# Kernel tuning notes

Measured on AMD Instinct MI355X. Metric: run time of the kernel, lower is better.

The kernel has to match this reference:

```python
import jax, jax.numpy as jnp
import numpy as np

D = 512       # d_model
DC = 768      # d_context
H = 8         # heads
DFF = 2048    # d_ff
EPS = 1e-6


def _ln(x, g, b):
    mu = jnp.mean(x, axis=-1, keepdims=True)
    var = jnp.mean(jnp.square(x - mu), axis=-1, keepdims=True)
    return (x - mu) * jax.lax.rsqrt(var + EPS) * g + b


def _mha(q_in, k_in, v_in, mask, wq, bq, wk, bk, wv, bv, wo, bo):
    # q_in [B,Sq,D], k_in/v_in [B,Sk,D], mask [B,Sq,Sk] (nonzero -> blocked)
    B, Sq, _ = q_in.shape
    Sk = k_in.shape[1]
    dh = D // H
    q = (q_in @ wq + bq).reshape(B, Sq, H, dh)
    k = (k_in @ wk + bk).reshape(B, Sk, H, dh)
    v = (v_in @ wv + bv).reshape(B, Sk, H, dh)
    scores = jnp.einsum('bqhd,bkhd->bhqk', q, k) / np.float32(np.sqrt(dh))
    scores = jnp.where(mask[:, None, :, :].astype(bool), jnp.float32(-1e18), scores)
    attn = jax.nn.softmax(scores, axis=-1)
    ctx = jnp.einsum('bhqk,bkhd->bqhd', attn, v).reshape(B, Sq, D)
    return ctx @ wo + bo


def _aggregate_chains(batch_size, ctx_out, chain_map, chain_mask):
    # ctx_out [TC,S,D]; keep positions where mask[:,:,0] is set, else -inf,
    # then max-pool chains belonging to the same example (segment max).
    keep = chain_mask[:, :, 0].astype(bool)[:, :, None]
    masked = jnp.where(keep, ctx_out, jnp.float32(-jnp.inf))
    out = jax.ops.segment_max(masked, chain_map, num_segments=batch_size)
    # replicate torch.where(out + 1 == out, 0, out): zeros out -inf entries
    return jnp.where(out + 1 == out, jnp.float32(0.0), out)


def _lin_params(key, din, dout):
    return jax.random.normal(key, (din, dout), jnp.float32) * 0.02, jnp.zeros((dout,), jnp.float32)


def setup_inputs() -> dict:
    key = jax.random.key(0)
    ks = jax.random.split(key, 20)
    B, S, TC, L = 16, 512, 128, 12
    inp = {}
    inp['inputs'] = jax.random.normal(ks[0], (B, S, D), jnp.float32)
    inp['attn_mask'] = jax.random.randint(ks[1], (B, S, S), 0, 2, jnp.int32)
    inp['chain_map'] = jax.random.randint(ks[2], (TC,), 0, B, jnp.int32)
    inp['span_embeddings'] = jax.random.normal(ks[3], (TC, L, DC), jnp.float32)
    inp['chain_mask'] = jax.random.randint(ks[4], (TC, S, L), 0, 2, jnp.int32)
    inp['ln_g'] = jnp.ones((D,), jnp.float32)
    inp['ln_b'] = jnp.zeros((D,), jnp.float32)
    inp['sa_wq'], inp['sa_bq'] = _lin_params(ks[5], D, D)
    inp['sa_wk'], inp['sa_bk'] = _lin_params(ks[6], D, D)
    inp['sa_wv'], inp['sa_bv'] = _lin_params(ks[7], D, D)
    inp['sa_wo'], inp['sa_bo'] = _lin_params(ks[8], D, D)
    inp['lc_w'], inp['lc_b'] = _lin_params(ks[9], DC, D)
    inp['ca_wq'], inp['ca_bq'] = _lin_params(ks[10], D, D)
    inp['ca_wk'], inp['ca_bk'] = _lin_params(ks[11], D, D)
    inp['ca_wv'], inp['ca_bv'] = _lin_params(ks[12], D, D)
    inp['ca_wo'], inp['ca_bo'] = _lin_params(ks[13], D, D)
    inp['g_w'], inp['g_b'] = _lin_params(ks[14], 2 * D, D)
    inp['ff_ln_g'] = jnp.ones((D,), jnp.float32)
    inp['ff_ln_b'] = jnp.zeros((D,), jnp.float32)
    inp['ff_w1'], inp['ff_b1'] = _lin_params(ks[15], D, DFF)
    inp['ff_w2'], inp['ff_b2'] = _lin_params(ks[16], DFF, D)
    return inp


def reference(inputs, attn_mask, chain_map, span_embeddings, chain_mask,
              ln_g, ln_b,
              sa_wq, sa_bq, sa_wk, sa_bk, sa_wv, sa_bv, sa_wo, sa_bo,
              lc_w, lc_b,
              ca_wq, ca_bq, ca_wk, ca_bk, ca_wv, ca_bv, ca_wo, ca_bo,
              g_w, g_b,
              ff_ln_g, ff_ln_b, ff_w1, ff_b1, ff_w2, ff_b2):
    B = inputs.shape[0]
    input_norm = _ln(inputs, ln_g, ln_b)
    attn_context = _mha(input_norm, input_norm, input_norm, attn_mask,
                        sa_wq, sa_bq, sa_wk, sa_bk, sa_wv, sa_bv, sa_wo, sa_bo)
    emb_transformed = span_embeddings @ lc_w + lc_b              # [TC,L,D]
    context_query = input_norm[chain_map]                         # [TC,S,D]
    ctx_out = _mha(context_query, emb_transformed, emb_transformed, chain_mask,
                   ca_wq, ca_bq, ca_wk, ca_bk, ca_wv, ca_bv, ca_wo, ca_bo)
    ctx_context = _aggregate_chains(B, ctx_out, chain_map, chain_mask)
    # SimpleGate
    z = jax.nn.sigmoid(jnp.concatenate((attn_context, ctx_context), axis=-1) @ g_w + g_b)
    gated = z * attn_context + (1.0 - z) * ctx_context
    out = gated + inputs  # dropout is identity at eval
    # PositionwiseFeedForward (pre-LN, residual)
    y = _ln(out, ff_ln_g, ff_ln_b)
    inter = jax.nn.relu(y @ ff_w1 + ff_b1)
    return inter @ ff_w2 + ff_b2 + out
```

## Files before the change

### kernel.cpp

```cpp
#include <hip/hip_runtime.h>
#include <hip/hip_bf16.h>
#include <math.h>

typedef float f32x4_t __attribute__((ext_vector_type(4)));
typedef __bf16 bf16x8_t __attribute__((ext_vector_type(8)));
typedef __bf16 bf16x4_t __attribute__((ext_vector_type(4)));

__device__ __forceinline__ void gload16(const void* g, void* l) {
  __builtin_amdgcn_global_load_lds((const __attribute__((address_space(1))) void*)g,
                                   (__attribute__((address_space(3))) void*)l, 16, 0, 0);
}

struct WDesc { const float* src; __bf16* hi; __bf16* lo; int K; int N; };
struct WPack { WDesc w[12]; };

__global__ __launch_bounds__(256) void prep_weights_kernel(WPack p) {
  WDesc d = p.w[blockIdx.y];
  const int tilesN = d.N >> 6;
  const int ntiles = (d.K >> 6) * tilesN;
  __shared__ float tile[64][65];
  const int tid = threadIdx.x;
  const int r = tid >> 4, cq = (tid & 15) << 2;
  const int c = tid >> 4, rq = (tid & 15) << 2;
  for (int t = blockIdx.x; t < ntiles; t += gridDim.x) {
    const int tk = t / tilesN, tn = t - tk * tilesN;
    const int k0 = tk << 6, n0 = tn << 6;
#pragma unroll
    for (int i = 0; i < 4; i++) {
      const float4 v = *reinterpret_cast<const float4*>(
          &d.src[(size_t)(k0 + r + i * 16) * d.N + n0 + cq]);
      tile[r + i * 16][cq] = v.x; tile[r + i * 16][cq + 1] = v.y;
      tile[r + i * 16][cq + 2] = v.z; tile[r + i * 16][cq + 3] = v.w;
    }
    __syncthreads();
#pragma unroll
    for (int i = 0; i < 4; i++) {
      const int cc = c + i * 16;
      const float v0 = tile[rq][cc], v1 = tile[rq + 1][cc];
      const float v2 = tile[rq + 2][cc], v3 = tile[rq + 3][cc];
      const __bf16 h0 = (__bf16)v0, h1 = (__bf16)v1, h2 = (__bf16)v2, h3 = (__bf16)v3;
      bf16x4_t hv = {h0, h1, h2, h3};
      bf16x4_t lv = {(__bf16)(v0 - (float)h0), (__bf16)(v1 - (float)h1),
                     (__bf16)(v2 - (float)h2), (__bf16)(v3 - (float)h3)};
      *reinterpret_cast<bf16x4_t*>(&d.hi[(size_t)(n0 + cc) * d.K + k0 + rq]) = hv;
      *reinterpret_cast<bf16x4_t*>(&d.lo[(size_t)(n0 + cc) * d.K + k0 + rq]) = lv;
    }
    __syncthreads();
  }
}

__global__ __launch_bounds__(256) void bias_cat_kernel(
    const float* __restrict__ b0, const float* __restrict__ b1,
    const float* __restrict__ b2, const float* __restrict__ b3,
    float* __restrict__ out) {
  const int t = blockIdx.x * 256 + threadIdx.x;
  const float* s = t < 512 ? b0 : t < 1024 ? b1 : t < 1536 ? b2 : b3;
  out[t] = s[t & 511];
}

__global__ __launch_bounds__(256) void split_kernel(
    const float* __restrict__ x, __bf16* __restrict__ h, __bf16* __restrict__ l, int nq) {
  const int i = blockIdx.x * 256 + threadIdx.x;
  if (i >= nq) return;
  const float4 v = reinterpret_cast<const float4*>(x)[i];
  const __bf16 h0 = (__bf16)v.x, h1 = (__bf16)v.y, h2 = (__bf16)v.z, h3 = (__bf16)v.w;
  bf16x4_t hv = {h0, h1, h2, h3};
  bf16x4_t lv = {(__bf16)(v.x - (float)h0), (__bf16)(v.y - (float)h1),
                 (__bf16)(v.z - (float)h2), (__bf16)(v.w - (float)h3)};
  reinterpret_cast<bf16x4_t*>(h)[i] = hv;
  reinterpret_cast<bf16x4_t*>(l)[i] = lv;
}

__global__ __launch_bounds__(256) void ln_split_kernel(
    const float* __restrict__ x, const float* __restrict__ g,
    const float* __restrict__ bb, __bf16* __restrict__ yh, __bf16* __restrict__ yl) {
  const int row = blockIdx.x * 4 + (threadIdx.x >> 6);
  const int lane = threadIdx.x & 63;
  const float* xr = x + (size_t)row * 512;
  float4 a = *reinterpret_cast<const float4*>(&xr[lane * 8]);
  float4 b4 = *reinterpret_cast<const float4*>(&xr[lane * 8 + 4]);
  float v[8] = {a.x, a.y, a.z, a.w, b4.x, b4.y, b4.z, b4.w};
  float s = 0.f;
#pragma unroll
  for (int j = 0; j < 8; j++) s += v[j];
#pragma unroll
  for (int off = 1; off < 64; off <<= 1) s += __shfl_xor(s, off);
  const float mean = s * (1.f / 512.f);
  float sq = 0.f;
#pragma unroll
  for (int j = 0; j < 8; j++) { v[j] -= mean; sq += v[j] * v[j]; }
#pragma unroll
  for (int off = 1; off < 64; off <<= 1) sq += __shfl_xor(sq, off);
  const float inv = rsqrtf(sq * (1.f / 512.f) + 1e-6f);
  bf16x8_t hv, lv;
#pragma unroll
  for (int j = 0; j < 8; j++) {
    const float o = v[j] * inv * g[lane * 8 + j] + bb[lane * 8 + j];
    const __bf16 h = (__bf16)o;
    hv[j] = h; lv[j] = (__bf16)(o - (float)h);
  }
  *reinterpret_cast<bf16x8_t*>(&yh[(size_t)row * 512 + lane * 8]) = hv;
  *reinterpret_cast<bf16x8_t*>(&yl[(size_t)row * 512 + lane * 8]) = lv;
}

template <int EPI>
__global__ __launch_bounds__(256, 2) void gemm2_kernel(
    const __bf16* __restrict__ A0h, const __bf16* __restrict__ A0l,
    const __bf16* __restrict__ A1h, const __bf16* __restrict__ A1l,
    int lda, int ksplit,
    const __bf16* __restrict__ Bh, const __bf16* __restrict__ Bl, int K,
    const float* __restrict__ bias,
    float* __restrict__ Cf, __bf16* __restrict__ Ch, __bf16* __restrict__ Cl,
    __bf16* __restrict__ C2h, __bf16* __restrict__ C2l,
    __bf16* __restrict__ C3h, __bf16* __restrict__ C3l,
    int ldc, size_t sec_stride,
    const __bf16* __restrict__ e0h, const __bf16* __restrict__ e0l,
    const __bf16* __restrict__ e1h, const __bf16* __restrict__ e1l,
    const float* __restrict__ e2) {
  __shared__ __bf16 lds[4][128][64];
  const int tid = threadIdx.x;
  const int wave = tid >> 6, lane = tid & 63;
  const int brow = blockIdx.y * 128, bcol = blockIdx.x * 128;
  const int wr = (wave >> 1) * 64, wc = (wave & 1) * 64;
  const int lr = lane & 15, hi = lane >> 4;
  const int s_row = lane >> 3;
  const int s_sc = (lane & 7) ^ s_row;
  const int tile_row = (wave < 2 ? brow : bcol) + s_row;

  f32x4_t acc[4][4] = {};

  for (int k0 = 0; k0 < K; k0 += 64) {
    const __bf16* ah = A0h; const __bf16* al = A0l; int kc = k0;
    if (k0 >= ksplit) { ah = A1h; al = A1l; kc = k0 - ksplit; }
    const __bf16* plane = wave == 0 ? ah : wave == 1 ? al : wave == 2 ? Bh : Bl;
    const int pl_lda = wave < 2 ? lda : K;
    const int pk = wave < 2 ? kc : k0;
    const __bf16* src = plane + (size_t)tile_row * pl_lda + pk + s_sc * 8;
#pragma unroll
    for (int i = 0; i < 16; i++)
      gload16(src + (size_t)i * 8 * pl_lda, &lds[wave][i * 8][0]);
    __syncthreads();
#pragma unroll
    for (int kk = 0; kk < 2; kk++) {
      bf16x8_t afh[4], afl[4], bfh[4], bfl[4];
#pragma unroll
      for (int m = 0; m < 4; m++) {
        const int row = wr + m * 16 + lr;
        const int ch = (kk * 4 + hi) ^ (row & 7);
        afh[m] = *(const bf16x8_t*)((const char*)&lds[0][0][0] + row * 128 + ch * 16);
        afl[m] = *(const bf16x8_t*)((const char*)&lds[1][0][0] + row * 128 + ch * 16);
      }
#pragma unroll
      for (int n = 0; n < 4; n++) {
        const int row = wc + n * 16 + lr;
        const int ch = (kk * 4 + hi) ^ (row & 7);
        bfh[n] = *(const bf16x8_t*)((const char*)&lds[2][0][0] + row * 128 + ch * 16);
        bfl[n] = *(const bf16x8_t*)((const char*)&lds[3][0][0] + row * 128 + ch * 16);
      }
#pragma unroll
      for (int m = 0; m < 4; m++)
#pragma unroll
        for (int n = 0; n < 4; n++) {
          acc[m][n] = __builtin_amdgcn_mfma_f32_16x16x32_bf16(afh[m], bfh[n], acc[m][n], 0, 0, 0);
          acc[m][n] = __builtin_amdgcn_mfma_f32_16x16x32_bf16(afh[m], bfl[n], acc[m][n], 0, 0, 0);
          acc[m][n] = __builtin_amdgcn_mfma_f32_16x16x32_bf16(afl[m], bfh[n], acc[m][n], 0, 0, 0);
        }
    }
    __syncthreads();
  }

#pragma unroll
  for (int m = 0; m < 4; m++) {
#pragma unroll
    for (int n = 0; n < 4; n++) {
      const int colg = bcol + wc + n * 16 + lr;
      const size_t cb = (size_t)(colg >> 9) * sec_stride + (colg & 511);
      const float bv = bias[colg];
#pragma unroll
      for (int r = 0; r < 4; r++) {
        const int row = brow + wr + m * 16 + hi * 4 + r;
        float v = acc[m][n][r] + bv;
        if constexpr (EPI == 0) {
          Cf[cb + (size_t)row * ldc] = v;
        } else if constexpr (EPI == 1) {
          const __bf16 h = (__bf16)v;
          Ch[cb + (size_t)row * ldc] = h;
          Cl[cb + (size_t)row * ldc] = (__bf16)(v - (float)h);
        } else if constexpr (EPI == 2) {
          v = fmaxf(v, 0.f);
          const __bf16 h = (__bf16)v;
          Ch[cb + (size_t)row * ldc] = h;
          Cl[cb + (size_t)row * ldc] = (__bf16)(v - (float)h);
        } else if constexpr (EPI == 3) {
          const float z = 1.f / (1.f + expf(-v));
          const size_t ei = (size_t)row * 512 + colg;
          const float a = (float)e0h[ei] + (float)e0l[ei];
          const float c = (float)e1h[ei] + (float)e1l[ei];
          Cf[cb + (size_t)row * ldc] = z * a + (1.f - z) * c + e2[ei];
        } else if constexpr (EPI == 4) {
          Cf[cb + (size_t)row * ldc] = v + e2[(size_t)row * 512 + colg];
        } else if constexpr (EPI == 5) {
          const int sec = colg >> 9, cc = colg & 511;
          const __bf16 h = (__bf16)v;
          const __bf16 lo = (__bf16)(v - (float)h);
          if (sec == 0)      { Ch[(size_t)row * 512 + cc] = h;  Cl[(size_t)row * 512 + cc] = lo; }
          else if (sec == 1) { C2h[(size_t)row * 512 + cc] = h; C2l[(size_t)row * 512 + cc] = lo; }
          else if (sec == 2) {
            const int bb2 = row >> 9, ss = row & 511, hh2 = cc >> 6, dv = cc & 63;
            const size_t va = ((size_t)((bb2 * 8 + hh2) * 64 + dv)) * 512 + ss;
            C3h[va] = h; C3l[va] = lo;
          } else {
            Cf[(size_t)row * 512 + cc] = v;
          }
        }
      }
    }
  }
}

__global__ __launch_bounds__(256, 2) void sa_attn_mfma_kernel(
    const __bf16* __restrict__ Qh_g, const __bf16* __restrict__ Ql_g,
    const __bf16* __restrict__ Kh_g, const __bf16* __restrict__ Kl_g,
    const __bf16* __restrict__ Vth_g, const __bf16* __restrict__ Vtl_g,
    const int* __restrict__ mask,
    __bf16* __restrict__ Oh, __bf16* __restrict__ Ol) {
  __shared__ __bf16 Qs[2][64][64];
  __shared__ __bf16 Ks[2][64][64];
  __shared__ __bf16 Vs[2][64][64];
  __shared__ __bf16 Ps[2][64][64];
  const int tid = threadIdx.x;
  const int wid = tid >> 6, lane = tid & 63;
  const int q0 = blockIdx.x * 64;
  const int h = blockIdx.y, b = blockIdx.z;
  const int lr = lane & 15, hi = lane >> 4;
  const int s_row = lane >> 3;
  const int s_sc = (lane & 7) ^ s_row;

  {
    const __bf16* qp = (wid < 2 ? Qh_g : Ql_g);
    const int pl = (wid < 2 ? 0 : 1);
    const int r0 = (wid & 1) * 32;
    const __bf16* src = qp + (size_t)(b * 512 + q0 + r0 + s_row) * 512 + h * 64 + s_sc * 8;
#pragma unroll
    for (int i = 0; i < 4; i++)
      gload16(src + (size_t)i * 8 * 512, &Qs[pl][r0 + i * 8][0]);
  }
  f32x4_t accO[4] = {};
  float m_[4], l_[4];
#pragma unroll
  for (int j = 0; j < 4; j++) { m_[j] = -INFINITY; l_[j] = 0.f; }

  for (int kt = 0; kt < 8; kt++) {
    const int k0 = kt * 64;
    __syncthreads();
    {
      const __bf16* plane = wid == 0 ? Kh_g : wid == 1 ? Kl_g : wid == 2 ? Vth_g : Vtl_g;
      size_t srow; int scol;
      if (wid < 2) { srow = (size_t)(b * 512 + k0 + s_row);          scol = h * 64; }
      else         { srow = (size_t)((b * 8 + h) * 64 + s_row);      scol = k0; }
      const __bf16* src = plane + srow * 512 + scol + s_sc * 8;
      __bf16* dst0 = (wid == 0) ? &Ks[0][0][0] : (wid == 1) ? &Ks[1][0][0]
                   : (wid == 2) ? &Vs[0][0][0] : &Vs[1][0][0];
#pragma unroll
      for (int i = 0; i < 8; i++)
        gload16(src + (size_t)i * 8 * 512, dst0 + i * 8 * 64);
    }
    __syncthreads();

    f32x4_t acc[4] = {};
#pragma unroll
    for (int kk = 0; kk < 2; kk++) {
      const int arow = wid * 16 + lr;
      const int ach = (kk * 4 + hi) ^ (arow & 7);
      bf16x8_t aqh = *(const bf16x8_t*)&Qs[0][arow][ach * 8];
      bf16x8_t aql = *(const bf16x8_t*)&Qs[1][arow][ach * 8];
#pragma unroll
      for (int n = 0; n < 4; n++) {
        const int brw = n * 16 + lr;
        const int bch = (kk * 4 + hi) ^ (brw & 7);
        bf16x8_t bkh = *(const bf16x8_t*)&Ks[0][brw][bch * 8];
        bf16x8_t bkl = *(const bf16x8_t*)&Ks[1][brw][bch * 8];
        acc[n] = __builtin_amdgcn_mfma_f32_16x16x32_bf16(aqh, bkh, acc[n], 0, 0, 0);
        acc[n] = __builtin_amdgcn_mfma_f32_16x16x32_bf16(aqh, bkl, acc[n], 0, 0, 0);
        acc[n] = __builtin_amdgcn_mfma_f32_16x16x32_bf16(aql, bkh, acc[n], 0, 0, 0);
      }
    }

    float p[4][4];
    const int qbase = b * 512 + q0 + wid * 16 + hi * 4;
#pragma unroll
    for (int j = 0; j < 4; j++) {
      float rowmax = -INFINITY;
#pragma unroll
      for (int n = 0; n < 4; n++) {
        const int mk = mask[(size_t)(qbase + j) * 512 + k0 + n * 16 + lr];
        const float sv = mk ? -1e18f : acc[n][j] * 0.125f;
        p[n][j] = sv;
        rowmax = fmaxf(rowmax, sv);
      }
#pragma unroll
      for (int off = 1; off <= 8; off <<= 1) rowmax = fmaxf(rowmax, __shfl_xor(rowmax, off));
      const float mnew = fmaxf(m_[j], rowmax);
      const float scale = expf(m_[j] - mnew);
      float rs = 0.f;
#pragma unroll
      for (int n = 0; n < 4; n++) { const float e = expf(p[n][j] - mnew); p[n][j] = e; rs += e; }
#pragma unroll
      for (int off = 1; off <= 8; off <<= 1) rs += __shfl_xor(rs, off);
      l_[j] = l_[j] * scale + rs;
      m_[j] = mnew;
#pragma unroll
      for (int nv = 0; nv < 4; nv++) accO[nv][j] *= scale;
    }

#pragma unroll
    for (int j = 0; j < 4; j++) {
      const int qrow = wid * 16 + hi * 4 + j;
#pragma unroll
      for (int n = 0; n < 4; n++) {
        const int col = n * 16 + lr;
        const int colp = ((((col >> 3) ^ (qrow & 7)) << 3) | (col & 7));
        const __bf16 ph = (__bf16)p[n][j];
        Ps[0][qrow][colp] = ph;
        Ps[1][qrow][colp] = (__bf16)(p[n][j] - (float)ph);
      }
    }

#pragma unroll
    for (int kk = 0; kk < 2; kk++) {
      const int arow = wid * 16 + lr;
      const int ach = (kk * 4 + hi) ^ (arow & 7);
      bf16x8_t aph = *(const bf16x8_t*)&Ps[0][arow][ach * 8];
      bf16x8_t apl = *(const bf16x8_t*)&Ps[1][arow][ach * 8];
#pragma unroll
      for (int nv = 0; nv < 4; nv++) {
        const int brw = nv * 16 + lr;
        const int bch = (kk * 4 + hi) ^ (brw & 7);
        bf16x8_t bvh = *(const bf16x8_t*)&Vs[0][brw][bch * 8];
        bf16x8_t bvl = *(const bf16x8_t*)&Vs[1][brw][bch * 8];
        accO[nv] = __builtin_amdgcn_mfma_f32_16x16x32_bf16(aph, bvh, accO[nv], 0, 0, 0);
        accO[nv] = __builtin_amdgcn_mfma_f32_16x16x32_bf16(aph, bvl, accO[nv], 0, 0, 0);
        accO[nv] = __builtin_amdgcn_mfma_f32_16x16x32_bf16(apl, bvh, accO[nv], 0, 0, 0);
      }
    }
  }

#pragma unroll
  for (int j = 0; j < 4; j++) {
    const float inv = 1.f / l_[j];
    const size_t orow = (size_t)(b * 512 + q0 + wid * 16 + hi * 4 + j) * 512 + h * 64;
#pragma unroll
    for (int nv = 0; nv < 4; nv++) {
      const float o = accO[nv][j] * inv;
      const __bf16 hh = (__bf16)o;
      Oh[orow + nv * 16 + lr] = hh;
      Ol[orow + nv * 16 + lr] = (__bf16)(o - (float)hh);
    }
  }
}

__global__ __launch_bounds__(256) void ca_attn_kernel(
    const float* __restrict__ Qbase, const float* __restrict__ Kc,
    const float* __restrict__ Vc, const int* __restrict__ chain_map,
    const int* __restrict__ chain_mask,
    __bf16* __restrict__ Oh, __bf16* __restrict__ Ol, int c0) {
  __shared__ float ks[12][512];
  __shared__ float vs[12][512];
  const int tid = threadIdx.x;
  const int cl = blockIdx.y, c = c0 + cl, s0 = blockIdx.x * 32;
#pragma unroll
  for (int i = 0; i < 6; i++) {
    const int fi = i * 256 + tid;
    const int lrow = fi >> 7, dq = (fi & 127) << 2;
    *reinterpret_cast<float4*>(&ks[lrow][dq]) =
        *reinterpret_cast<const float4*>(&Kc[((size_t)c * 12 + lrow) * 512 + dq]);
    *reinterpret_cast<float4*>(&vs[lrow][dq]) =
        *reinterpret_cast<const float4*>(&Vc[((size_t)c * 12 + lrow) * 512 + dq]);
  }
  __syncthreads();
  const int h = tid >> 5, sl = tid & 31;
  const int s = s0 + sl;
  const int bq = chain_map[c];
  const float* qrow = &Qbase[((size_t)(bq * 512 + s)) * 512 + h * 64];
  float4 q4[16];
#pragma unroll
  for (int i = 0; i < 16; i++) q4[i] = *reinterpret_cast<const float4*>(&qrow[i * 4]);
  const int* mrow = &chain_mask[((size_t)(c * 512 + s)) * 12];
  float sc[12];
  float mx = -INFINITY;
#pragma unroll
  for (int lI = 0; lI < 12; lI++) {
    float acc = 0.f;
#pragma unroll
    for (int i = 0; i < 16; i++) {
      const float4 kv = *reinterpret_cast<const float4*>(&ks[lI][h * 64 + i * 4]);
      acc += q4[i].x * kv.x + q4[i].y * kv.y + q4[i].z * kv.z + q4[i].w * kv.w;
    }
    acc *= 0.125f;
    if (mrow[lI]) acc = -1e18f;
    sc[lI] = acc;
    mx = fmaxf(mx, acc);
  }
  float sum = 0.f;
#pragma unroll
  for (int lI = 0; lI < 12; lI++) { sc[lI] = expf(sc[lI] - mx); sum += sc[lI]; }
  const float inv = 1.f / sum;
  const size_t obase = ((size_t)(cl * 512 + s)) * 512 + h * 64;
#pragma unroll
  for (int dq = 0; dq < 16; dq++) {
    float4 ov = make_float4(0.f, 0.f, 0.f, 0.f);
#pragma unroll
    for (int lI = 0; lI < 12; lI++) {
      const float4 vv = *reinterpret_cast<const float4*>(&vs[lI][h * 64 + dq * 4]);
      ov.x += sc[lI] * vv.x; ov.y += sc[lI] * vv.y;
      ov.z += sc[lI] * vv.z; ov.w += sc[lI] * vv.w;
    }
    float vo[4] = {ov.x * inv, ov.y * inv, ov.z * inv, ov.w * inv};
    bf16x4_t hv, lv;
#pragma unroll
    for (int j = 0; j < 4; j++) {
      const __bf16 hh = (__bf16)vo[j];
      hv[j] = hh; lv[j] = (__bf16)(vo[j] - (float)hh);
    }
    *reinterpret_cast<bf16x4_t*>(&Oh[obase + dq * 4]) = hv;
    *reinterpret_cast<bf16x4_t*>(&Ol[obase + dq * 4]) = lv;
  }
}

template <int MODE>
__global__ __launch_bounds__(256) void agg2_kernel(
    const float* __restrict__ ctxB, const int* __restrict__ chain_map,
    const int* __restrict__ chain_mask,
    __bf16* __restrict__ ch, __bf16* __restrict__ cl, int c0) {
  const int s = blockIdx.x, b = blockIdx.y, tid = threadIdx.x;
  const size_t orow = ((size_t)(b * 512 + s)) * 512;
  float v0 = -3.0e38f, v1 = -3.0e38f;
  if (MODE != 0) {
    v0 = (float)ch[orow + tid] + (float)cl[orow + tid];
    v1 = (float)ch[orow + 256 + tid] + (float)cl[orow + 256 + tid];
  }
  for (int i = 0; i < 16; i++) {
    const int c = c0 + i;
    if (chain_map[c] == b && chain_mask[((size_t)(c * 512 + s)) * 12] != 0) {
      const float* row = &ctxB[((size_t)(i * 512 + s)) * 512];
      v0 = fmaxf(v0, row[tid]);
      v1 = fmaxf(v1, row[tid + 256]);
    }
  }
  if (MODE == 2) {
    if (v0 < -1.0e38f) v0 = 0.f;
    if (v1 < -1.0e38f) v1 = 0.f;
  }
  const __bf16 h0 = (__bf16)v0, h1 = (__bf16)v1;
  ch[orow + tid] = h0;        cl[orow + tid] = (__bf16)(v0 - (float)h0);
  ch[orow + 256 + tid] = h1;  cl[orow + 256 + tid] = (__bf16)(v1 - (float)h1);
}

extern "C" void kernel_launch(void* const* d_in, const int* in_sizes, int n_in,
                              void* d_out, int out_size, void* d_ws, size_t ws_size,
                              hipStream_t stream) {
  const float* inputs     = (const float*)d_in[0];
  const int*   attn_mask  = (const int*)d_in[1];
  const int*   chain_map  = (const int*)d_in[2];
  const float* span       = (const float*)d_in[3];
  const int*   chain_mask = (const int*)d_in[4];
  const float* ln_g = (const float*)d_in[5];
  const float* ln_b = (const float*)d_in[6];
  const float* sa_bq = (const float*)d_in[8];
  const float* sa_bk = (const float*)d_in[10];
  const float* sa_bv = (const float*)d_in[12];
  const float* sa_bo = (const float*)d_in[14];
  const float* lc_b  = (const float*)d_in[16];
  const float* ca_bq = (const float*)d_in[18];
  const float* ca_bk = (const float*)d_in[20];
  const float* ca_bv = (const float*)d_in[22];
  const float* ca_bo = (const float*)d_in[24];
  const float* g_b   = (const float*)d_in[26];
  const float* ff_ln_g = (const float*)d_in[27];
  const float* ff_ln_b = (const float*)d_in[28];
  const float* ff_b1 = (const float*)d_in[30];
  const float* ff_b2 = (const float*)d_in[32];

  char* ws = (char*)d_ws;
  size_t off = 0;
  auto alloc = [&](size_t bytes) -> void* {
    off = (off + 255) & ~(size_t)255;
    void* p = ws + off;
    off += bytes;
    return p;
  };

  const size_t wel[9] = {2048ull*512, 768ull*512, 512ull*512, 512ull*512,
                         512ull*512, 512ull*512, 1024ull*512, 512ull*2048, 2048ull*512};
  __bf16* WH[9]; __bf16* WL[9];
  for (int i = 0; i < 9; i++) {
    WH[i] = (__bf16*)alloc(wel[i] * 2);
    WL[i] = (__bf16*)alloc(wel[i] * 2);
  }
  WPack pack;
  pack.w[0] = {(const float*)d_in[7],  WH[0],               WL[0],               512, 512};
  pack.w[1] = {(const float*)d_in[9],  WH[0] + 512*512,     WL[0] + 512*512,     512, 512};
  pack.w[2] = {(const float*)d_in[11], WH[0] + 1024*512,    WL[0] + 1024*512,    512, 512};
  pack.w[3] = {(const float*)d_in[17], WH[0] + 1536*512,    WL[0] + 1536*512,    512, 512};
  pack.w[4] = {(const float*)d_in[15], WH[1], WL[1], 768, 512};
  pack.w[5] = {(const float*)d_in[19], WH[2], WL[2], 512, 512};
  pack.w[6] = {(const float*)d_in[21], WH[3], WL[3], 512, 512};
  pack.w[7] = {(const float*)d_in[13], WH[4], WL[4], 512, 512};
  pack.w[8] = {(const float*)d_in[23], WH[5], WL[5], 512, 512};
  pack.w[9] = {(const float*)d_in[25], WH[6], WL[6], 1024, 512};
  pack.w[10] = {(const float*)d_in[29], WH[7], WL[7], 512, 2048};
  pack.w[11] = {(const float*)d_in[31], WH[8], WL[8], 2048, 512};

  float* bias_cat = (float*)alloc(2048 * 4);

  const size_t E_BSD = 8192ull * 512;
  char* R_A = (char*)alloc(E_BSD * 4);
  char* R_B = (char*)alloc(E_BSD * 16);
  __bf16* spanh = (__bf16*)alloc(1536ull * 768 * 2);
  __bf16* spanl = (__bf16*)alloc(1536ull * 768 * 2);
  __bf16* embh  = (__bf16*)alloc(1536ull * 512 * 2);
  __bf16* embl  = (__bf16*)alloc(1536ull * 512 * 2);
  float*  v_ca  = (float*)alloc(1536ull * 512 * 4);
  if (ws_size < off) return;

  __bf16* xh = (__bf16*)R_A;           __bf16* xl = xh + E_BSD;
  __bf16* sh = xh;                     __bf16* sl = xl;
  __bf16* cah = xh;                    __bf16* cal = xl;
  float*  out1 = (float*)R_A;
  __bf16* Qh_g = (__bf16*)R_B;                    __bf16* Ql_g = Qh_g + E_BSD;
  __bf16* Kh_g = (__bf16*)(R_B + E_BSD * 4);      __bf16* Kl_g = Kh_g + E_BSD;
  __bf16* VTh_g = (__bf16*)(R_B + E_BSD * 8);     __bf16* VTl_g = VTh_g + E_BSD;
  float*  caQ  = (float*)(R_B + E_BSD * 12);
  float*  ctxB  = (float*)R_B;
  __bf16* ah_pl = (__bf16*)(R_B + E_BSD * 4);     __bf16* al_pl = ah_pl + E_BSD;
  __bf16* cth   = (__bf16*)(R_B + E_BSD * 8);     __bf16* ctl   = cth + E_BSD;
  __bf16* yh    = (__bf16*)(R_B + E_BSD * 12);    __bf16* yl    = yh + E_BSD;
  __bf16* ih    = (__bf16*)R_B;                   __bf16* il    = ih + 4096ull * 2048;
  float* k_ca = (float*)spanh;
  float* dout = (float*)d_out;
  const int KBIG = 1 << 30;
  const float* Z = nullptr;
  const __bf16* ZB = nullptr;
  __bf16* ZM = nullptr;

  auto gemm = [&](int EPI, const __bf16* a0h, const __bf16* a0l,
                  const __bf16* a1h, const __bf16* a1l, int lda, int ksplit,
                  int wi, int K, const float* bias,
                  float* cf, __bf16* chp, __bf16* clp,
                  __bf16* c2h, __bf16* c2l, __bf16* c3h, __bf16* c3l,
                  int ldc, size_t secs,
                  const __bf16* E0h, const __bf16* E0l,
                  const __bf16* E1h, const __bf16* E1l, const float* E2,
                  int M, int N) {
    dim3 grid(N / 128, M / 128);
    switch (EPI) {
      case 0: gemm2_kernel<0><<<grid, 256, 0, stream>>>(a0h, a0l, a1h, a1l, lda, ksplit, WH[wi], WL[wi], K, bias, cf, chp, clp, c2h, c2l, c3h, c3l, ldc, secs, E0h, E0l, E1h, E1l, E2); break;
      case 1: gemm2_kernel<1><<<grid, 256, 0, stream>>>(a0h, a0l, a1h, a1l, lda, ksplit, WH[wi], WL[wi], K, bias, cf, chp, clp, c2h, c2l, c3h, c3l, ldc, secs, E0h, E0l, E1h, E1l, E2); break;
      case 2: gemm2_kernel<2><<<grid, 256, 0, stream>>>(a0h, a0l, a1h, a1l, lda, ksplit, WH[wi], WL[wi], K, bias, cf, chp, clp, c2h, c2l, c3h, c3l, ldc, secs, E0h, E0l, E1h, E1l, E2); break;
      case 3: gemm2_kernel<3><<<grid, 256, 0, stream>>>(a0h, a0l, a1h, a1l, lda, ksplit, WH[wi], WL[wi], K, bias, cf, chp, clp, c2h, c2l, c3h, c3l, ldc, secs, E0h, E0l, E1h, E1l, E2); break;
      case 4: gemm2_kernel<4><<<grid, 256, 0, stream>>>(a0h, a0l, a1h, a1l, lda, ksplit, WH[wi], WL[wi], K, bias, cf, chp, clp, c2h, c2l, c3h, c3l, ldc, secs, E0h, E0l, E1h, E1l, E2); break;
      case 5: gemm2_kernel<5><<<grid, 256, 0, stream>>>(a0h, a0l, a1h, a1l, lda, ksplit, WH[wi], WL[wi], K, bias, cf, chp, clp, c2h, c2l, c3h, c3l, ldc, secs, E0h, E0l, E1h, E1l, E2); break;
    }
  };

  prep_weights_kernel<<<dim3(64, 12), 256, 0, stream>>>(pack);
  bias_cat_kernel<<<8, 256, 0, stream>>>(sa_bq, sa_bk, sa_bv, ca_bq, bias_cat);
  split_kernel<<<1152, 256, 0, stream>>>(span, spanh, spanl, 1536 * 768 / 4);
  ln_split_kernel<<<2048, 256, 0, stream>>>(inputs, ln_g, ln_b, xh, xl);

  gemm(5, xh, xl, xh, xl, 512, KBIG, 0, 512, bias_cat,
       caQ, Qh_g, Ql_g, Kh_g, Kl_g, VTh_g, VTl_g, 512, 0,
       ZB, ZB, ZB, ZB, Z, 8192, 2048);

  sa_attn_mfma_kernel<<<dim3(8, 8, 16), 256, 0, stream>>>(
      Qh_g, Ql_g, Kh_g, Kl_g, VTh_g, VTl_g, attn_mask, sh, sl);
  gemm(1, sh, sl, sh, sl, 512, KBIG, 4, 512, sa_bo,
       nullptr, ah_pl, al_pl, ZM, ZM, ZM, ZM, 512, 0, ZB, ZB, ZB, ZB, Z, 8192, 512);

  gemm(1, spanh, spanl, spanh, spanl, 768, KBIG, 1, 768, lc_b,
       nullptr, embh, embl, ZM, ZM, ZM, ZM, 512, 0, ZB, ZB, ZB, ZB, Z, 1536, 512);
  gemm(0, embh, embl, embh, embl, 512, KBIG, 2, 512, ca_bk,
       k_ca, nullptr, nullptr, ZM, ZM, ZM, ZM, 512, 0, ZB, ZB, ZB, ZB, Z, 1536, 512);
  gemm(0, embh, embl, embh, embl, 512, KBIG, 3, 512, ca_bv,
       v_ca, nullptr, nullptr, ZM, ZM, ZM, ZM, 512, 0, ZB, ZB, ZB, ZB, Z, 1536, 512);

  for (int chk = 0; chk < 8; chk++) {
    const int c0 = chk * 16;
    ca_attn_kernel<<<dim3(16, 16), 256, 0, stream>>>(caQ, k_ca, v_ca, chain_map, chain_mask, cah, cal, c0);
    gemm(0, cah, cal, cah, cal, 512, KBIG, 5, 512, ca_bo,
         ctxB, nullptr, nullptr, ZM, ZM, ZM, ZM, 512, 0, ZB, ZB, ZB, ZB, Z, 8192, 512);
    if (chk == 0)      agg2_kernel<0><<<dim3(512, 16), 256, 0, stream>>>(ctxB, chain_map, chain_mask, cth, ctl, c0);
    else if (chk == 7) agg2_kernel<2><<<dim3(512, 16), 256, 0, stream>>>(ctxB, chain_map, chain_mask, cth, ctl, c0);
    else               agg2_kernel<1><<<dim3(512, 16), 256, 0, stream>>>(ctxB, chain_map, chain_mask, cth, ctl, c0);
  }

  gemm(3, ah_pl, al_pl, cth, ctl, 512, 512, 6, 1024, g_b,
       out1, nullptr, nullptr, ZM, ZM, ZM, ZM, 512, 0,
       ah_pl, al_pl, cth, ctl, inputs, 8192, 512);

  ln_split_kernel<<<2048, 256, 0, stream>>>(out1, ff_ln_g, ff_ln_b, yh, yl);
  for (int r0 = 0; r0 < 8192; r0 += 4096) {
    gemm(2, yh + (size_t)r0 * 512, yl + (size_t)r0 * 512,
         yh + (size_t)r0 * 512, yl + (size_t)r0 * 512, 512, KBIG, 7, 512, ff_b1,
         nullptr, ih, il, ZM, ZM, ZM, ZM, 2048, 512, ZB, ZB, ZB, ZB, Z, 4096, 2048);
    gemm(4, ih, il, ih, il, 2048, KBIG, 8, 2048, ff_b2,
         dout + (size_t)r0 * 512, nullptr, nullptr, ZM, ZM, ZM, ZM, 512, 0,
         ZB, ZB, ZB, ZB, out1 + (size_t)r0 * 512, 4096, 512);
  }
}
```

Baseline: 1.196 ms.

## Fuse chain max-aggregation into output GEMM via atomicMax and widen GEMM to 512 threads

Replaces the separate per-chunk aggregation kernel, and the fp32 ctxB round trip it needed, with a GEMM epilogue. The epilogue encodes each masked output as an order-preserving unsigned int and applies atomicMax into a pre-filled buffer. A final decode kernel converts that buffer back to hi/lo bf16 and zeroes entries that were never written. Separately, all GEMMs now launch 512 threads, with each of 8 waves computing a 64x32 subtile, to raise wave-level parallelism. The costs are atomic contention on global memory and an extra fill and decode pass over the aggregation buffer.

```diff
diff --git a/kernel.cpp b/kernel.cpp
--- a/kernel.cpp
+++ b/kernel.cpp
@@ -71,6 +71,29 @@
   reinterpret_cast<bf16x4_t*>(l)[i] = lv;
 }
 
+__global__ __launch_bounds__(256) void fill_umax_kernel(unsigned* __restrict__ p) {
+  const unsigned e = ~__float_as_uint(-3.0e38f);
+  reinterpret_cast<uint4*>(p)[blockIdx.x * 256 + threadIdx.x] = make_uint4(e, e, e, e);
+}
+
+__global__ __launch_bounds__(256) void decode_umax_kernel(
+    const unsigned* __restrict__ u, __bf16* __restrict__ ch, __bf16* __restrict__ cl) {
+  const int i = blockIdx.x * 256 + threadIdx.x;
+  const uint4 v = reinterpret_cast<const uint4*>(u)[i];
+  unsigned a[4] = {v.x, v.y, v.z, v.w};
+  bf16x4_t hv, lv;
+#pragma unroll
+  for (int j = 0; j < 4; j++) {
+    const unsigned bits = (a[j] & 0x80000000u) ? (a[j] & 0x7FFFFFFFu) : ~a[j];
+    float f = __uint_as_float(bits);
+    if (f < -1.0e38f) f = 0.f;
+    const __bf16 hh = (__bf16)f;
+    hv[j] = hh; lv[j] = (__bf16)(f - (float)hh);
+  }
+  reinterpret_cast<bf16x4_t*>(ch)[i] = hv;
+  reinterpret_cast<bf16x4_t*>(cl)[i] = lv;
+}
+
 __global__ __launch_bounds__(256) void ln_split_kernel(
     const float* __restrict__ x, const float* __restrict__ g,
     const float* __restrict__ bb, __bf16* __restrict__ yh, __bf16* __restrict__ yl) {
@@ -104,7 +127,7 @@
 }
 
 template <int EPI>
-__global__ __launch_bounds__(256, 2) void gemm2_kernel(
+__global__ __launch_bounds__(512, 4) void gemm2_kernel(
     const __bf16* __restrict__ A0h, const __bf16* __restrict__ A0l,
     const __bf16* __restrict__ A1h, const __bf16* __restrict__ A1l,
     int lda, int ksplit,
@@ -116,33 +139,37 @@
     int ldc, size_t sec_stride,
     const __bf16* __restrict__ e0h, const __bf16* __restrict__ e0l,
     const __bf16* __restrict__ e1h, const __bf16* __restrict__ e1l,
-    const float* __restrict__ e2) {
+    const float* __restrict__ e2,
+    const int* __restrict__ cmap, const int* __restrict__ cmask, int c0) {
   __shared__ __bf16 lds[4][128][64];
   const int tid = threadIdx.x;
   const int wave = tid >> 6, lane = tid & 63;
   const int brow = blockIdx.y * 128, bcol = blockIdx.x * 128;
-  const int wr = (wave >> 1) * 64, wc = (wave & 1) * 64;
+  const int wr = (wave >> 2) * 64, wc = (wave & 3) * 32;
   const int lr = lane & 15, hi = lane >> 4;
   const int s_row = lane >> 3;
   const int s_sc = (lane & 7) ^ s_row;
-  const int tile_row = (wave < 2 ? brow : bcol) + s_row;
-
-  f32x4_t acc[4][4] = {};
+  const int pl_id = wave >> 1;
+  const int half = (wave & 1) * 64;
+  const int trow_base = (pl_id < 2 ? brow : bcol) + half;
+
+  f32x4_t acc[4][2] = {};
 
   for (int k0 = 0; k0 < K; k0 += 64) {
     const __bf16* ah = A0h; const __bf16* al = A0l; int kc = k0;
     if (k0 >= ksplit) { ah = A1h; al = A1l; kc = k0 - ksplit; }
-    const __bf16* plane = wave == 0 ? ah : wave == 1 ? al : wave == 2 ? Bh : Bl;
-    const int pl_lda = wave < 2 ? lda : K;
-    const int pk = wave < 2 ? kc : k0;
-    const __bf16* src = plane + (size_t)tile_row * pl_lda + pk + s_sc * 8;
-#pragma unroll
-    for (int i = 0; i < 16; i++)
-      gload16(src + (size_t)i * 8 * pl_lda, &lds[wave][i * 8][0]);
+    const __bf16* plane = pl_id == 0 ? ah : pl_id == 1 ? al : pl_id == 2 ? Bh : Bl;
+    const int pl_lda = pl_id < 2 ? lda : K;
+    const int pk = pl_id < 2 ? kc : k0;
+    const __bf16* src = plane + (size_t)(trow_base + s_row) * pl_lda + pk + s_sc * 8;
+    __bf16* ldst = &lds[pl_id][half][0];
+#pragma unroll
+    for (int i = 0; i < 8; i++)
+      gload16(src + (size_t)i * 8 * pl_lda, ldst + i * 8 * 64);
     __syncthreads();
 #pragma unroll
     for (int kk = 0; kk < 2; kk++) {
-      bf16x8_t afh[4], afl[4], bfh[4], bfl[4];
+      bf16x8_t afh[4], afl[4], bfh[2], bfl[2];
 #pragma unroll
       for (int m = 0; m < 4; m++) {
         const int row = wr + m * 16 + lr;
@@ -151,7 +178,7 @@
         afl[m] = *(const bf16x8_t*)((const char*)&lds[1][0][0] + row * 128 + ch * 16);
       }
 #pragma unroll
-      for (int n = 0; n < 4; n++) {
+      for (int n = 0; n < 2; n++) {
         const int row = wc + n * 16 + lr;
         const int ch = (kk * 4 + hi) ^ (row & 7);
         bfh[n] = *(const bf16x8_t*)((const char*)&lds[2][0][0] + row * 128 + ch * 16);
@@ -160,7 +187,7 @@
 #pragma unroll
       for (int m = 0; m < 4; m++)
 #pragma unroll
-        for (int n = 0; n < 4; n++) {
+        for (int n = 0; n < 2; n++) {
           acc[m][n] = __builtin_amdgcn_mfma_f32_16x16x32_bf16(afh[m], bfh[n], acc[m][n], 0, 0, 0);
           acc[m][n] = __builtin_amdgcn_mfma_f32_16x16x32_bf16(afh[m], bfl[n], acc[m][n], 0, 0, 0);
           acc[m][n] = __builtin_amdgcn_mfma_f32_16x16x32_bf16(afl[m], bfh[n], acc[m][n], 0, 0, 0);
@@ -172,7 +199,7 @@
 #pragma unroll
   for (int m = 0; m < 4; m++) {
 #pragma unroll
-    for (int n = 0; n < 4; n++) {
+    for (int n = 0; n < 2; n++) {
       const int colg = bcol + wc + n * 16 + lr;
       const size_t cb = (size_t)(colg >> 9) * sec_stride + (colg & 511);
       const float bv = bias[colg];
@@ -212,6 +239,14 @@
           } else {
             Cf[(size_t)row * 512 + cc] = v;
           }
+        } else if constexpr (EPI == 6) {
+          const int clc = row >> 9, s = row & 511;
+          if (cmask[((size_t)((c0 + clc) * 512 + s)) * 12] != 0) {
+            const int b = cmap[c0 + clc];
+            const unsigned bits = __float_as_uint(v);
+            const unsigned enc = (bits & 0x80000000u) ? ~bits : (bits | 0x80000000u);
+            atomicMax((unsigned*)Cf + ((size_t)(b * 512 + s)) * 512 + colg, enc);
+          }
         }
       }
     }
@@ -256,8 +291,8 @@
     {
       const __bf16* plane = wid == 0 ? Kh_g : wid == 1 ? Kl_g : wid == 2 ? Vth_g : Vtl_g;
       size_t srow; int scol;
-      if (wid < 2) { srow = (size_t)(b * 512 + k0 + s_row);          scol = h * 64; }
-      else         { srow = (size_t)((b * 8 + h) * 64 + s_row);      scol = k0; }
+      if (wid < 2) { srow = (size_t)(b * 512 + k0 + s_row);     scol = h * 64; }
+      else         { srow = (size_t)((b * 8 + h) * 64 + s_row); scol = k0; }
       const __bf16* src = plane + srow * 512 + scol + s_sc * 8;
       __bf16* dst0 = (wid == 0) ? &Ks[0][0][0] : (wid == 1) ? &Ks[1][0][0]
                    : (wid == 2) ? &Vs[0][0][0] : &Vs[1][0][0];
@@ -425,35 +460,6 @@
     *reinterpret_cast<bf16x4_t*>(&Oh[obase + dq * 4]) = hv;
     *reinterpret_cast<bf16x4_t*>(&Ol[obase + dq * 4]) = lv;
   }
-}
-
-template <int MODE>
-__global__ __launch_bounds__(256) void agg2_kernel(
-    const float* __restrict__ ctxB, const int* __restrict__ chain_map,
-    const int* __restrict__ chain_mask,
-    __bf16* __restrict__ ch, __bf16* __restrict__ cl, int c0) {
-  const int s = blockIdx.x, b = blockIdx.y, tid = threadIdx.x;
-  const size_t orow = ((size_t)(b * 512 + s)) * 512;
-  float v0 = -3.0e38f, v1 = -3.0e38f;
-  if (MODE != 0) {
-    v0 = (float)ch[orow + tid] + (float)cl[orow + tid];
-    v1 = (float)ch[orow + 256 + tid] + (float)cl[orow + 256 + tid];
-  }
-  for (int i = 0; i < 16; i++) {
-    const int c = c0 + i;
-    if (chain_map[c] == b && chain_mask[((size_t)(c * 512 + s)) * 12] != 0) {
-      const float* row = &ctxB[((size_t)(i * 512 + s)) * 512];
-      v0 = fmaxf(v0, row[tid]);
-      v1 = fmaxf(v1, row[tid + 256]);
-    }
-  }
-  if (MODE == 2) {
-    if (v0 < -1.0e38f) v0 = 0.f;
-    if (v1 < -1.0e38f) v1 = 0.f;
-  }
-  const __bf16 h0 = (__bf16)v0, h1 = (__bf16)v1;
-  ch[orow + tid] = h0;        cl[orow + tid] = (__bf16)(v0 - (float)h0);
-  ch[orow + 256 + tid] = h1;  cl[orow + 256 + tid] = (__bf16)(v1 - (float)h1);
 }
 
 extern "C" void kernel_launch(void* const* d_in, const int* in_sizes, int n_in,
@@ -523,15 +529,15 @@
   float*  v_ca  = (float*)alloc(1536ull * 512 * 4);
   if (ws_size < off) return;
 
-  __bf16* xh = (__bf16*)R_A;           __bf16* xl = xh + E_BSD;
-  __bf16* sh = xh;                     __bf16* sl = xl;
-  __bf16* cah = xh;                    __bf16* cal = xl;
-  float*  out1 = (float*)R_A;
+  __bf16* xh = (__bf16*)R_A;   __bf16* xl = xh + E_BSD;
+  __bf16* sh = xh;             __bf16* sl = xl;
+  unsigned* umax = (unsigned*)R_A;
+  float* out1 = (float*)R_A;
   __bf16* Qh_g = (__bf16*)R_B;                    __bf16* Ql_g = Qh_g + E_BSD;
   __bf16* Kh_g = (__bf16*)(R_B + E_BSD * 4);      __bf16* Kl_g = Kh_g + E_BSD;
   __bf16* VTh_g = (__bf16*)(R_B + E_BSD * 8);     __bf16* VTl_g = VTh_g + E_BSD;
   float*  caQ  = (float*)(R_B + E_BSD * 12);
-  float*  ctxB  = (float*)R_B;
+  __bf16* cah = (__bf16*)R_B;                     __bf16* cal = cah + E_BSD;
   __bf16* ah_pl = (__bf16*)(R_B + E_BSD * 4);     __bf16* al_pl = ah_pl + E_BSD;
   __bf16* cth   = (__bf16*)(R_B + E_BSD * 8);     __bf16* ctl   = cth + E_BSD;
   __bf16* yh    = (__bf16*)(R_B + E_BSD * 12);    __bf16* yl    = yh + E_BSD;
@@ -551,15 +557,16 @@
                   int ldc, size_t secs,
                   const __bf16* E0h, const __bf16* E0l,
                   const __bf16* E1h, const __bf16* E1l, const float* E2,
-                  int M, int N) {
+                  int M, int N, const int* cmap, const int* cmask, int c0) {
     dim3 grid(N / 128, M / 128);
     switch (EPI) {
-      case 0: gemm2_kernel<0><<<grid, 256, 0, stream>>>(a0h, a0l, a1h, a1l, lda, ksplit, WH[wi], WL[wi], K, bias, cf, chp, clp, c2h, c2l, c3h, c3l, ldc, secs, E0h, E0l, E1h, E1l, E2); break;
-      case 1: gemm2_kernel<1><<<grid, 256, 0, stream>>>(a0h, a0l, a1h, a1l, lda, ksplit, WH[wi], WL[wi], K, bias, cf, chp, clp, c2h, c2l, c3h, c3l, ldc, secs, E0h, E0l, E1h, E1l, E2); break;
-      case 2: gemm2_kernel<2><<<grid, 256, 0, stream>>>(a0h, a0l, a1h, a1l, lda, ksplit, WH[wi], WL[wi], K, bias, cf, chp, clp, c2h, c2l, c3h, c3l, ldc, secs, E0h, E0l, E1h, E1l, E2); break;
-      case 3: gemm2_kernel<3><<<grid, 256, 0, stream>>>(a0h, a0l, a1h, a1l, lda, ksplit, WH[wi], WL[wi], K, bias, cf, chp, clp, c2h, c2l, c3h, c3l, ldc, secs, E0h, E0l, E1h, E1l, E2); break;
-      case 4: gemm2_kernel<4><<<grid, 256, 0, stream>>>(a0h, a0l, a1h, a1l, lda, ksplit, WH[wi], WL[wi], K, bias, cf, chp, clp, c2h, c2l, c3h, c3l, ldc, secs, E0h, E0l, E1h, E1l, E2); break;
-      case 5: gemm2_kernel<5><<<grid, 256, 0, stream>>>(a0h, a0l, a1h, a1l, lda, ksplit, WH[wi], WL[wi], K, bias, cf, chp, clp, c2h, c2l, c3h, c3l, ldc, secs, E0h, E0l, E1h, E1l, E2); break;
+      case 0: gemm2_kernel<0><<<grid, 512, 0, stream>>>(a0h, a0l, a1h, a1l, lda, ksplit, WH[wi], WL[wi], K, bias, cf, chp, clp, c2h, c2l, c3h, c3l, ldc, secs, E0h, E0l, E1h, E1l, E2, cmap, cmask, c0); break;
+      case 1: gemm2_kernel<1><<<grid, 512, 0, stream>>>(a0h, a0l, a1h, a1l, lda, ksplit, WH[wi], WL[wi], K, bias, cf, chp, clp, c2h, c2l, c3h, c3l, ldc, secs, E0h, E0l, E1h, E1l, E2, cmap, cmask, c0); break;
+      case 2: gemm2_kernel<2><<<grid, 512, 0, stream>>>(a0h, a0l, a1h, a1l, lda, ksplit, WH[wi], WL[wi], K, bias, cf, chp, clp, c2h, c2l, c3h, c3l, ldc, secs, E0h, E0l, E1h, E1l, E2, cmap, cmask, c0); break;
+      case 3: gemm2_kernel<3><<<grid, 512, 0, stream>>>(a0h, a0l, a1h, a1l, lda, ksplit, WH[wi], WL[wi], K, bias, cf, chp, clp, c2h, c2l, c3h, c3l, ldc, secs, E0h, E0l, E1h, E1l, E2, cmap, cmask, c0); break;
+      case 4: gemm2_kernel<4><<<grid, 512, 0, stream>>>(a0h, a0l, a1h, a1l, lda, ksplit, WH[wi], WL[wi], K, bias, cf, chp, clp, c2h, c2l, c3h, c3l, ldc, secs, E0h, E0l, E1h, E1l, E2, cmap, cmask, c0); break;
+      case 5: gemm2_kernel<5><<<grid, 512, 0, stream>>>(a0h, a0l, a1h, a1l, lda, ksplit, WH[wi], WL[wi], K, bias, cf, chp, clp, c2h, c2l, c3h, c3l, ldc, secs, E0h, E0l, E1h, E1l, E2, cmap, cmask, c0); break;
+      case 6: gemm2_kernel<6><<<grid, 512, 0, stream>>>(a0h, a0l, a1h, a1l, lda, ksplit, WH[wi], WL[wi], K, bias, cf, chp, clp, c2h, c2l, c3h, c3l, ldc, secs, E0h, E0l, E1h, E1l, E2, cmap, cmask, c0); break;
     }
   };
 
@@ -570,41 +577,46 @@
 
   gemm(5, xh, xl, xh, xl, 512, KBIG, 0, 512, bias_cat,
        caQ, Qh_g, Ql_g, Kh_g, Kl_g, VTh_g, VTl_g, 512, 0,
-       ZB, ZB, ZB, ZB, Z, 8192, 2048);
+       ZB, ZB, ZB, ZB, Z, 8192, 2048, nullptr, nullptr, 0);
 
   sa_attn_mfma_kernel<<<dim3(8, 8, 16), 256, 0, stream>>>(
       Qh_g, Ql_g, Kh_g, Kl_g, VTh_g, VTl_g, attn_mask, sh, sl);
   gemm(1, sh, sl, sh, sl, 512, KBIG, 4, 512, sa_bo,
-       nullptr, ah_pl, al_pl, ZM, ZM, ZM, ZM, 512, 0, ZB, ZB, ZB, ZB, Z, 8192, 512);
+       nullptr, ah_pl, al_pl, ZM, ZM, ZM, ZM, 512, 0, ZB, ZB, ZB, ZB, Z,
+       8192, 512, nullptr, nullptr, 0);
+  fill_umax_kernel<<<4096, 256, 0, stream>>>(umax);
 
   gemm(1, spanh, spanl, spanh, spanl, 768, KBIG, 1, 768, lc_b,
-       nullptr, embh, embl, ZM, ZM, ZM, ZM, 512, 0, ZB, ZB, ZB, ZB, Z, 1536, 512);
+       nullptr, embh, embl, ZM, ZM, ZM, ZM, 512, 0, ZB, ZB, ZB, ZB, Z,
+       1536, 512, nullptr, nullptr, 0);
   gemm(0, embh, embl, embh, embl, 512, KBIG, 2, 512, ca_bk,
-       k_ca, nullptr, nullptr, ZM, ZM, ZM, ZM, 512, 0, ZB, ZB, ZB, ZB, Z, 1536, 512);
+       k_ca, nullptr, nullptr, ZM, ZM, ZM, ZM, 512, 0, ZB, ZB, ZB, ZB, Z,
+       1536, 512, nullptr, nullptr, 0);
   gemm(0, embh, embl, embh, embl, 512, KBIG, 3, 512, ca_bv,
-       v_ca, nullptr, nullptr, ZM, ZM, ZM, ZM, 512, 0, ZB, ZB, ZB, ZB, Z, 1536, 512);
+       v_ca, nullptr, nullptr, ZM, ZM, ZM, ZM, 512, 0, ZB, ZB, ZB, ZB, Z,
+       1536, 512, nullptr, nullptr, 0);
 
   for (int chk = 0; chk < 8; chk++) {
     const int c0 = chk * 16;
     ca_attn_kernel<<<dim3(16, 16), 256, 0, stream>>>(caQ, k_ca, v_ca, chain_map, chain_mask, cah, cal, c0);
-    gemm(0, cah, cal, cah, cal, 512, KBIG, 5, 512, ca_bo,
-         ctxB, nullptr, nullptr, ZM, ZM, ZM, ZM, 512, 0, ZB, ZB, ZB, ZB, Z, 8192, 512);
-    if (chk == 0)      agg2_kernel<0><<<dim3(512, 16), 256, 0, stream>>>(ctxB, chain_map, chain_mask, cth, ctl, c0);
-    else if (chk == 7) agg2_kernel<2><<<dim3(512, 16), 256, 0, stream>>>(ctxB, chain_map, chain_mask, cth, ctl, c0);
-    else               agg2_kernel<1><<<dim3(512, 16), 256, 0, stream>>>(ctxB, chain_map, chain_mask, cth, ctl, c0);
-  }
+    gemm(6, cah, cal, cah, cal, 512, KBIG, 5, 512, ca_bo,
+         (float*)umax, nullptr, nullptr, ZM, ZM, ZM, ZM, 512, 0,
+         ZB, ZB, ZB, ZB, Z, 8192, 512, chain_map, chain_mask, c0);
+  }
+  decode_umax_kernel<<<4096, 256, 0, stream>>>(umax, cth, ctl);
 
   gemm(3, ah_pl, al_pl, cth, ctl, 512, 512, 6, 1024, g_b,
        out1, nullptr, nullptr, ZM, ZM, ZM, ZM, 512, 0,
-       ah_pl, al_pl, cth, ctl, inputs, 8192, 512);
+       ah_pl, al_pl, cth, ctl, inputs, 8192, 512, nullptr, nullptr, 0);
 
   ln_split_kernel<<<2048, 256, 0, stream>>>(out1, ff_ln_g, ff_ln_b, yh, yl);
   for (int r0 = 0; r0 < 8192; r0 += 4096) {
     gemm(2, yh + (size_t)r0 * 512, yl + (size_t)r0 * 512,
          yh + (size_t)r0 * 512, yl + (size_t)r0 * 512, 512, KBIG, 7, 512, ff_b1,
-         nullptr, ih, il, ZM, ZM, ZM, ZM, 2048, 512, ZB, ZB, ZB, ZB, Z, 4096, 2048);
+         nullptr, ih, il, ZM, ZM, ZM, ZM, 2048, 512, ZB, ZB, ZB, ZB, Z,
+         4096, 2048, nullptr, nullptr, 0);
     gemm(4, ih, il, ih, il, 2048, KBIG, 8, 2048, ff_b2,
          dout + (size_t)r0 * 512, nullptr, nullptr, ZM, ZM, ZM, ZM, 512, 0,
-         ZB, ZB, ZB, ZB, out1 + (size_t)r0 * 512, 4096, 512);
-  }
-}
+         ZB, ZB, ZB, ZB, out1 + (size_t)r0 * 512, 4096, 512, nullptr, nullptr, 0);
+  }
+}
```

Result: faster. 1.125 ms (-5.9%).
